# Optimization experiments

Measured on AMD Instinct MI355X. Metric: run time of the kernel, lower is better.

## Reference

```python
import jax, jax.numpy as jnp
import numpy as np

MASK_PENALTY = 1000.0
K = 1  # default k in bds_loss


def setup_inputs() -> dict:
    key = jax.random.key(0)
    k1, k2, k3, k4, k5, k6 = jax.random.split(key, 6)
    bt, nv, nf, H, W, S = 4, 20000, 40000, 256, 256, 2048
    verts = jax.random.normal(k1, (bt, nv, 3), dtype=jnp.float32)
    bds_xyz = jax.random.normal(k2, (bt, S, 3), dtype=jnp.float32)
    bds_mask = (jax.random.uniform(k3, (bt, S, 1)) < 0.7).astype(jnp.float32)
    bds = jnp.concatenate([bds_xyz, bds_mask], axis=-1)  # [bt,S,4]
    faces = jax.random.randint(k4, (bt, nf, 3), 0, nv, dtype=jnp.int64)
    p2f = jax.random.randint(k5, (bt, H, W, 1), 0, bt * nf, dtype=jnp.int64)
    bg = jax.random.uniform(k6, (bt, H, W, 1)) < 0.3
    pix_to_face = jnp.where(bg, jnp.int64(-1), p2f)
    return {"verts": verts, "bds": bds, "faces": faces,
            "pix_to_face": pix_to_face, "n_samples": S}


def _bds_loss(verts, bds, faces, pix_to_face, n_samples, k=K):
    bt, nv, _ = verts.shape
    # subsample boundary points (order-invariant -> identity indexing)
    bds_v = bds[:, :n_samples, :-1]   # [bt,S,3]
    bds_m = bds[:, :n_samples, -1]    # [bt,S]

    # ---- visibility mask from rasterized face indices ----
    fi = pix_to_face[..., 0].reshape(-1)                       # [bt*H*W]
    offs = jnp.arange(bt, dtype=faces.dtype)[:, None, None] * nv
    faces_packed = (faces + offs).reshape(-1, 3)               # [bt*nf,3]
    valid = fi >= 0
    fi_safe = jnp.where(valid, fi, 0)
    sel = faces_packed[fi_safe]                                # [bt*HW,3]
    vals = jnp.broadcast_to(valid[:, None], sel.shape).astype(verts.dtype)
    visible = jnp.zeros(bt * nv, dtype=verts.dtype).at[sel.reshape(-1)].max(vals.reshape(-1))
    visible = visible.reshape(bt, nv)                          # [bt,nv], 0/1

    # ---- squared pairwise distances: cdist(bds_v, verts)**2 ----
    d2 = (jnp.sum(bds_v * bds_v, -1)[:, :, None]
          + jnp.sum(verts * verts, -1)[:, None, :]
          - 2.0 * jnp.einsum('bsd,bvd->bsv', bds_v, verts))   # [bt,S,nv]

    dist = (1.0 - visible[:, None, :]) * MASK_PENALTY + visible[:, None, :] * d2
    min_dists = -jax.lax.top_k(-dist, k)[0]                    # [bt,S,k] smallest-k

    loss = (min_dists * bds_m[:, :, None]).mean(-1).sum(-1)    # [bt]
    return loss.mean()


def reference(verts, bds, faces, pix_to_face, n_samples):
    return _bds_loss(verts, bds, faces, pix_to_face, n_samples)
```

## Files before the change

kernel.cpp:

```cpp
#include <hip/hip_runtime.h>

#define BT   4
#define NV   20000
#define NF   40000
#define SMP  2048
#define NPIX (BT * 256 * 256)
#define NVG  (BT * NV)
#define NCH  128
#define CHUNK ((NV + NCH - 1) / NCH)
#define P    8
#define RED_BLOCKS 32

__global__ void init_k(float* __restrict__ visible,
                       int* __restrict__ flags,
                       float* __restrict__ acc,
                       unsigned int* __restrict__ cnt) {
    int i = blockIdx.x * blockDim.x + threadIdx.x;
    if (i < NVG) visible[i] = 0.0f;
    if (i < BT)  flags[i]   = 0;
    if (i == 0) { acc[0] = 0.0f; cnt[0] = 0u; }
}

__global__ void vis_k(const int4* __restrict__ p2f,
                      const int* __restrict__ faces,
                      float* __restrict__ visible) {
    int p = blockIdx.x * blockDim.x + threadIdx.x;
    int4 f4 = p2f[p];
    int fs[4] = {f4.x, f4.y, f4.z, f4.w};
    #pragma unroll
    for (int k = 0; k < 4; ++k) {
        int fi = fs[k];
        if (fi >= 0) {
            int b    = fi / NF;
            int base = fi * 3;
            int off  = b * NV;
            visible[faces[base + 0] + off] = 1.0f;
            visible[faces[base + 1] + off] = 1.0f;
            visible[faces[base + 2] + off] = 1.0f;
        }
    }
}

__global__ void pack_k(const float* __restrict__ verts,
                       const float* __restrict__ visible,
                       float4* __restrict__ packed,
                       int* __restrict__ flags) {
    int i = blockIdx.x * blockDim.x + threadIdx.x;
    if (i >= NVG) return;
    float x = verts[3 * i + 0];
    float y = verts[3 * i + 1];
    float z = verts[3 * i + 2];
    float w;
    if (visible[i] > 0.0f) {
        w = x * x + y * y + z * z;
    } else {
        w = 1e30f;
        flags[i / NV] = 1;
    }
    packed[i] = make_float4(-2.0f * x, -2.0f * y, -2.0f * z, w);
}

__global__ __launch_bounds__(256) void
main_k(const float4* __restrict__ bds,
       const float4* __restrict__ packed,
       float* __restrict__ mnOut) {
    __shared__ float4 sh[256];
    const int b  = blockIdx.z;
    const int c  = blockIdx.x;
    const int v0 = c * CHUNK;
    const int v1 = min(v0 + CHUNK, NV);

    float px[P], py[P], pz[P], mn[P];
    #pragma unroll
    for (int u = 0; u < P; ++u) {
        float4 p = bds[b * SMP + u * 256 + threadIdx.x];
        px[u] = p.x; py[u] = p.y; pz[u] = p.z;
        mn[u] = 3.0e38f;
    }

    const float4* vp = packed + b * NV;
    for (int t = v0; t < v1; t += 256) {
        int idx = t + threadIdx.x;
        if (idx < v1) sh[threadIdx.x] = vp[idx];
        __syncthreads();
        int cnt = min(256, v1 - t);
        #pragma unroll 4
        for (int j = 0; j < cnt; ++j) {
            float4 v = sh[j];
            #pragma unroll
            for (int u = 0; u < P; ++u) {
                float q = fmaf(px[u], v.x,
                          fmaf(py[u], v.y,
                          fmaf(pz[u], v.z, v.w)));
                mn[u] = fminf(mn[u], q);
            }
        }
        __syncthreads();
    }
    float* dst = mnOut + c * (BT * SMP) + b * SMP;
    #pragma unroll
    for (int u = 0; u < P; ++u)
        dst[u * 256 + threadIdx.x] = mn[u];
}

__global__ __launch_bounds__(256) void
red_k(const float* __restrict__ mnOut,
      const float4* __restrict__ bds,
      const int* __restrict__ flags,
      float* __restrict__ acc,
      unsigned int* __restrict__ cnt,
      float* __restrict__ out) {
    const int i = blockIdx.x * 256 + threadIdx.x;
    const int b = i >> 11;
    float4 p = bds[i];
    float v = mnOut[i];
    #pragma unroll 8
    for (int c = 1; c < NCH; ++c)
        v = fminf(v, mnOut[c * (BT * SMP) + i]);
    float bs = fmaf(p.x, p.x, fmaf(p.y, p.y, p.z * p.z));
    float mn = v + bs;
    if (flags[b]) mn = fminf(mn, 1000.0f);
    float contrib = mn * p.w;

    #pragma unroll
    for (int o = 32; o > 0; o >>= 1) contrib += __shfl_down(contrib, o, 64);
    __shared__ float part[4];
    if ((threadIdx.x & 63) == 0) part[threadIdx.x >> 6] = contrib;
    __syncthreads();
    if (threadIdx.x == 0) {
        float t = part[0] + part[1] + part[2] + part[3];
        atomicAdd(acc, t);
        __threadfence();
        unsigned int n = atomicAdd(cnt, 1u);
        if (n == RED_BLOCKS - 1) {
            __threadfence();
            out[0] = *((volatile float*)acc) / (float)BT;
        }
    }
}

extern "C" void kernel_launch(void* const* d_in, const int* in_sizes, int n_in,
                              void* d_out, int out_size, void* d_ws, size_t ws_size,
                              hipStream_t stream) {
    const float* verts = (const float*)d_in[0];
    const float* bds   = (const float*)d_in[1];
    const int*   faces = (const int*)d_in[2];
    const int*   p2f   = (const int*)d_in[3];
    float*       out   = (float*)d_out;

    char* ws = (char*)d_ws;
    float*  mnOut   = (float*)ws;
    float4* packed  = (float4*)(ws + 4194304);
    float*  visible = (float*)(ws + 4194304 + 1280000);
    int*    flags   = (int*)(ws + 4194304 + 1280000 + 320000);
    float*  acc     = (float*)(ws + 4194304 + 1280000 + 320016);
    unsigned int* cnt = (unsigned int*)(ws + 4194304 + 1280000 + 320020);

    init_k<<<(NVG + 255) / 256, 256, 0, stream>>>(visible, flags, acc, cnt);
    vis_k<<<(NPIX / 4 + 255) / 256, 256, 0, stream>>>(
        (const int4*)p2f, faces, visible);
    pack_k<<<(NVG + 255) / 256, 256, 0, stream>>>(verts, visible, packed, flags);
    main_k<<<dim3(NCH, 1, BT), 256, 0, stream>>>(
        (const float4*)bds, packed, mnOut);
    red_k<<<RED_BLOCKS, 256, 0, stream>>>(
        mnOut, (const float4*)bds, flags, acc, cnt, out);
}
```

Before: 112.2 us.

## Fuse all stages into one cooperative kernel with grid syncs

Replaces the five separate launches (init, visibility scatter, pack, distance-min, reduction) with a single cooperative kernel of 512 blocks that separates the phases with grid-wide syncs. Vertex packing now happens inside each block straight into shared memory for its chunk, so the packed buffer round trip is gone. The final reduction becomes a two-level scheme using per-block partials instead of atomics and a counter. It removes launch gaps and intermediate global traffic, but adds grid.sync costs and requires all 512 blocks to be co-resident.

```diff
diff --git a/kernel.cpp b/kernel.cpp
--- a/kernel.cpp
+++ b/kernel.cpp
@@ -1,4 +1,5 @@
 #include <hip/hip_runtime.h>
+#include <hip/hip_cooperative_groups.h>
 
 #define BT   4
 #define NV   20000
@@ -6,162 +7,162 @@
 #define SMP  2048
 #define NPIX (BT * 256 * 256)
 #define NVG  (BT * NV)
+#define NBLK 512
+#define NTH  256
 #define NCH  128
-#define CHUNK ((NV + NCH - 1) / NCH)
+#define CHUNK 157
 #define P    8
-#define RED_BLOCKS 32
 
-__global__ void init_k(float* __restrict__ visible,
-                       int* __restrict__ flags,
-                       float* __restrict__ acc,
-                       unsigned int* __restrict__ cnt) {
-    int i = blockIdx.x * blockDim.x + threadIdx.x;
-    if (i < NVG) visible[i] = 0.0f;
-    if (i < BT)  flags[i]   = 0;
-    if (i == 0) { acc[0] = 0.0f; cnt[0] = 0u; }
-}
+namespace cg = cooperative_groups;
 
-__global__ void vis_k(const int4* __restrict__ p2f,
-                      const int* __restrict__ faces,
-                      float* __restrict__ visible) {
-    int p = blockIdx.x * blockDim.x + threadIdx.x;
-    int4 f4 = p2f[p];
-    int fs[4] = {f4.x, f4.y, f4.z, f4.w};
-    #pragma unroll
-    for (int k = 0; k < 4; ++k) {
-        int fi = fs[k];
-        if (fi >= 0) {
-            int b    = fi / NF;
-            int base = fi * 3;
-            int off  = b * NV;
-            visible[faces[base + 0] + off] = 1.0f;
-            visible[faces[base + 1] + off] = 1.0f;
-            visible[faces[base + 2] + off] = 1.0f;
+__global__ __launch_bounds__(NTH) void fused_k(
+    const float*  __restrict__ verts,
+    const float4* __restrict__ bds,
+    const int*    __restrict__ faces,
+    const int4*   __restrict__ p2f,
+    float*        __restrict__ out,
+    float*        __restrict__ visible,
+    int*          __restrict__ flags,
+    float*        __restrict__ mnOut,
+    float*        __restrict__ partials)
+{
+    cg::grid_group grid = cg::this_grid();
+    const int tid  = threadIdx.x;
+    const int gid  = blockIdx.x;
+    const int gtid = gid * NTH + tid;
+
+    __shared__ float4 shv[CHUNK];
+    __shared__ float  shred[NTH];
+
+    if (gtid < NVG) visible[gtid] = 0.0f;
+    if (gtid < BT)  flags[gtid]   = 0;
+    grid.sync();
+
+    if (gtid < NPIX / 4) {
+        int4 f4 = p2f[gtid];
+        int fs[4] = {f4.x, f4.y, f4.z, f4.w};
+        #pragma unroll
+        for (int k = 0; k < 4; ++k) {
+            int fi = fs[k];
+            if (fi >= 0) {
+                int b    = fi / NF;
+                int base = fi * 3;
+                int off  = b * NV;
+                visible[faces[base + 0] + off] = 1.0f;
+                visible[faces[base + 1] + off] = 1.0f;
+                visible[faces[base + 2] + off] = 1.0f;
+            }
         }
     }
-}
+    grid.sync();
 
-__global__ void pack_k(const float* __restrict__ verts,
-                       const float* __restrict__ visible,
-                       float4* __restrict__ packed,
-                       int* __restrict__ flags) {
-    int i = blockIdx.x * blockDim.x + threadIdx.x;
-    if (i >= NVG) return;
-    float x = verts[3 * i + 0];
-    float y = verts[3 * i + 1];
-    float z = verts[3 * i + 2];
-    float w;
-    if (visible[i] > 0.0f) {
-        w = x * x + y * y + z * z;
-    } else {
-        w = 1e30f;
-        flags[i / NV] = 1;
-    }
-    packed[i] = make_float4(-2.0f * x, -2.0f * y, -2.0f * z, w);
-}
-
-__global__ __launch_bounds__(256) void
-main_k(const float4* __restrict__ bds,
-       const float4* __restrict__ packed,
-       float* __restrict__ mnOut) {
-    __shared__ float4 sh[256];
-    const int b  = blockIdx.z;
-    const int c  = blockIdx.x;
+    const int b  = gid >> 7;
+    const int c  = gid & (NCH - 1);
     const int v0 = c * CHUNK;
-    const int v1 = min(v0 + CHUNK, NV);
+    const int cnt = min(CHUNK, NV - v0);
 
     float px[P], py[P], pz[P], mn[P];
     #pragma unroll
     for (int u = 0; u < P; ++u) {
-        float4 p = bds[b * SMP + u * 256 + threadIdx.x];
+        float4 p = bds[b * SMP + u * NTH + tid];
         px[u] = p.x; py[u] = p.y; pz[u] = p.z;
         mn[u] = 3.0e38f;
     }
+    if (tid < cnt) {
+        int vi = b * NV + v0 + tid;
+        float x = verts[3 * vi + 0];
+        float y = verts[3 * vi + 1];
+        float z = verts[3 * vi + 2];
+        float w;
+        if (visible[vi] > 0.0f) {
+            w = x * x + y * y + z * z;
+        } else {
+            w = 1e30f;
+            flags[b] = 1;
+        }
+        shv[tid] = make_float4(-2.f * x, -2.f * y, -2.f * z, w);
+    }
+    __syncthreads();
+    #pragma unroll 4
+    for (int j = 0; j < cnt; ++j) {
+        float4 v = shv[j];
+        #pragma unroll
+        for (int u = 0; u < P; ++u) {
+            float q = fmaf(px[u], v.x,
+                      fmaf(py[u], v.y,
+                      fmaf(pz[u], v.z, v.w)));
+            mn[u] = fminf(mn[u], q);
+        }
+    }
+    {
+        float* dst = mnOut + (c * BT + b) * SMP;
+        #pragma unroll
+        for (int u = 0; u < P; ++u)
+            dst[u * NTH + tid] = mn[u];
+    }
+    grid.sync();
 
-    const float4* vp = packed + b * NV;
-    for (int t = v0; t < v1; t += 256) {
-        int idx = t + threadIdx.x;
-        if (idx < v1) sh[threadIdx.x] = vp[idx];
+    {
+        const int sloc = tid & 15;
+        const int cslc = tid >> 4;
+        const int i    = gid * 16 + sloc;
+        const int bb   = i >> 11;
+        const int ss   = i & (SMP - 1);
+        float v = 3.0e38f;
+        #pragma unroll
+        for (int k = 0; k < 8; ++k) {
+            int cc = cslc * 8 + k;
+            v = fminf(v, mnOut[(cc * BT + bb) * SMP + ss]);
+        }
+        shred[tid] = v;
         __syncthreads();
-        int cnt = min(256, v1 - t);
-        #pragma unroll 4
-        for (int j = 0; j < cnt; ++j) {
-            float4 v = sh[j];
+        float contrib = 0.0f;
+        if (tid < 16) {
+            float m = shred[tid];
             #pragma unroll
-            for (int u = 0; u < P; ++u) {
-                float q = fmaf(px[u], v.x,
-                          fmaf(py[u], v.y,
-                          fmaf(pz[u], v.z, v.w)));
-                mn[u] = fminf(mn[u], q);
-            }
+            for (int k = 1; k < 16; ++k) m = fminf(m, shred[tid + 16 * k]);
+            float4 p = bds[i];
+            float bs = fmaf(p.x, p.x, fmaf(p.y, p.y, p.z * p.z));
+            float mnv = m + bs;
+            if (flags[bb]) mnv = fminf(mnv, 1000.0f);
+            contrib = mnv * p.w;
         }
+        #pragma unroll
+        for (int o = 8; o > 0; o >>= 1)
+            contrib += __shfl_down(contrib, o, 64);
+        if (tid == 0) partials[gid] = contrib;
+    }
+    grid.sync();
+
+    if (gid == 0) {
+        float s = partials[tid] + partials[tid + NTH];
+        #pragma unroll
+        for (int o = 32; o > 0; o >>= 1) s += __shfl_down(s, o, 64);
+        if ((tid & 63) == 0) shred[tid >> 6] = s;
         __syncthreads();
-    }
-    float* dst = mnOut + c * (BT * SMP) + b * SMP;
-    #pragma unroll
-    for (int u = 0; u < P; ++u)
-        dst[u * 256 + threadIdx.x] = mn[u];
-}
-
-__global__ __launch_bounds__(256) void
-red_k(const float* __restrict__ mnOut,
-      const float4* __restrict__ bds,
-      const int* __restrict__ flags,
-      float* __restrict__ acc,
-      unsigned int* __restrict__ cnt,
-      float* __restrict__ out) {
-    const int i = blockIdx.x * 256 + threadIdx.x;
-    const int b = i >> 11;
-    float4 p = bds[i];
-    float v = mnOut[i];
-    #pragma unroll 8
-    for (int c = 1; c < NCH; ++c)
-        v = fminf(v, mnOut[c * (BT * SMP) + i]);
-    float bs = fmaf(p.x, p.x, fmaf(p.y, p.y, p.z * p.z));
-    float mn = v + bs;
-    if (flags[b]) mn = fminf(mn, 1000.0f);
-    float contrib = mn * p.w;
-
-    #pragma unroll
-    for (int o = 32; o > 0; o >>= 1) contrib += __shfl_down(contrib, o, 64);
-    __shared__ float part[4];
-    if ((threadIdx.x & 63) == 0) part[threadIdx.x >> 6] = contrib;
-    __syncthreads();
-    if (threadIdx.x == 0) {
-        float t = part[0] + part[1] + part[2] + part[3];
-        atomicAdd(acc, t);
-        __threadfence();
-        unsigned int n = atomicAdd(cnt, 1u);
-        if (n == RED_BLOCKS - 1) {
-            __threadfence();
-            out[0] = *((volatile float*)acc) / (float)BT;
-        }
+        if (tid == 0)
+            out[0] = (shred[0] + shred[1] + shred[2] + shred[3]) / (float)BT;
     }
 }
 
 extern "C" void kernel_launch(void* const* d_in, const int* in_sizes, int n_in,
                               void* d_out, int out_size, void* d_ws, size_t ws_size,
                               hipStream_t stream) {
-    const float* verts = (const float*)d_in[0];
-    const float* bds   = (const float*)d_in[1];
-    const int*   faces = (const int*)d_in[2];
-    const int*   p2f   = (const int*)d_in[3];
-    float*       out   = (float*)d_out;
+    const float*  verts = (const float*)d_in[0];
+    const float4* bds   = (const float4*)d_in[1];
+    const int*    faces = (const int*)d_in[2];
+    const int4*   p2f   = (const int4*)d_in[3];
+    float*        out   = (float*)d_out;
 
     char* ws = (char*)d_ws;
-    float*  mnOut   = (float*)ws;
-    float4* packed  = (float4*)(ws + 4194304);
-    float*  visible = (float*)(ws + 4194304 + 1280000);
-    int*    flags   = (int*)(ws + 4194304 + 1280000 + 320000);
-    float*  acc     = (float*)(ws + 4194304 + 1280000 + 320016);
-    unsigned int* cnt = (unsigned int*)(ws + 4194304 + 1280000 + 320020);
+    float* mnOut    = (float*)ws;
+    float* visible  = (float*)(ws + 4194304);
+    int*   flags    = (int*)(ws + 4194304 + 320000);
+    float* partials = (float*)(ws + 4194304 + 320000 + 64);
 
-    init_k<<<(NVG + 255) / 256, 256, 0, stream>>>(visible, flags, acc, cnt);
-    vis_k<<<(NPIX / 4 + 255) / 256, 256, 0, stream>>>(
-        (const int4*)p2f, faces, visible);
-    pack_k<<<(NVG + 255) / 256, 256, 0, stream>>>(verts, visible, packed, flags);
-    main_k<<<dim3(NCH, 1, BT), 256, 0, stream>>>(
-        (const float4*)bds, packed, mnOut);
-    red_k<<<RED_BLOCKS, 256, 0, stream>>>(
-        mnOut, (const float4*)bds, flags, acc, cnt, out);
+    void* args[] = { (void*)&verts, (void*)&bds, (void*)&faces, (void*)&p2f,
+                     (void*)&out, (void*)&visible, (void*)&flags,
+                     (void*)&mnOut, (void*)&partials };
+    hipLaunchCooperativeKernel((void*)fused_k, dim3(NBLK), dim3(NTH),
+                               args, 0, stream);
 }
```

New measurement: 303.1 us. 170% more time.
